# Kernel optimization log

Hardware: AMD Instinct MI355X
Metric: run time of the kernel (lower is better)

Reference implementation:

```python
import jax, jax.numpy as jnp
import numpy as np

DIM = 512
HEADS = 8
DIM_HEAD = 64
INNER = HEADS * DIM_HEAD  # 512


def setup_inputs() -> dict:
    key = jax.random.key(0)
    k1, k2, k3, k4 = jax.random.split(key, 4)
    x = jax.random.normal(k1, (2, 4096, DIM), dtype=jnp.float32)
    w_qkv = jax.random.normal(k2, (DIM, INNER * 3), dtype=jnp.float32) * (DIM ** -0.5)
    w_out = jax.random.normal(k3, (INNER, DIM), dtype=jnp.float32) * (INNER ** -0.5)
    b_out = jnp.zeros((DIM,), dtype=jnp.float32)
    temperature = jnp.asarray(np.log(DIM_HEAD ** -0.5), dtype=jnp.float32)
    return {"x": x, "w_qkv": w_qkv, "w_out": w_out, "b_out": b_out,
            "temperature": temperature}


def reference(x, w_qkv, w_out, b_out, temperature):
    b, n, _ = x.shape
    qkv = jnp.einsum('bnd,de->bne', x, w_qkv)            # [b,n,3*inner]
    q, k, v = jnp.split(qkv, 3, axis=-1)
    # 'b n (h d) -> b h n d'
    def to_heads(t):
        return t.reshape(b, n, HEADS, DIM_HEAD).transpose(0, 2, 1, 3)
    q, k, v = map(to_heads, (q, k, v))
    scale = jnp.exp(temperature)
    dots = jnp.einsum('bhid,bhjd->bhij', q, k) * scale   # [b,h,n,n]
    mask_value = -jnp.asarray(np.finfo(np.float32).max, dtype=dots.dtype)
    eye = jnp.eye(n, dtype=bool)
    dots = jnp.where(eye, mask_value, dots)
    attn = jax.nn.softmax(dots, axis=-1)
    out = jnp.einsum('bhij,bhjd->bhid', attn, v)         # [b,h,n,d]
    out = out.transpose(0, 2, 1, 3).reshape(b, n, INNER)  # 'b h n d -> b n (h d)'
    return jnp.einsum('bni,io->bno', out, w_out) + b_out
```

## Files before the change

kernel.cpp:

```cpp
#include <hip/hip_runtime.h>

typedef __bf16 bf16x8 __attribute__((ext_vector_type(8)));
typedef float  f32x4  __attribute__((ext_vector_type(4)));
typedef unsigned short u16;
typedef unsigned int   u32;

#define MFMA(a,b,c) __builtin_amdgcn_mfma_f32_16x16x32_bf16((a),(b),(c),0,0,0)

__device__ __forceinline__ u16 f2bf(float f){
    u32 u = __builtin_bit_cast(u32, f);
    u += 0x7FFFu + ((u >> 16) & 1u);
    return (u16)(u >> 16);
}

typedef __attribute__((address_space(3))) u32 lds32_t;
typedef __attribute__((address_space(1))) u32 glb32_t;

__device__ __forceinline__ void gll16(const u16* g, u16* l){
    __builtin_amdgcn_global_load_lds((const glb32_t*)g, (lds32_t*)l, 16, 0, 0);
}

__global__ __launch_bounds__(256) void cvt_x_kernel(const float* __restrict__ in,
                                                    u16* __restrict__ out, int n8){
    int i = blockIdx.x * 256 + threadIdx.x;
    if (i >= n8) return;
    const float4* p = (const float4*)in + (size_t)i * 2;
    float4 a = p[0], b = p[1];
    u16 r[8] = { f2bf(a.x), f2bf(a.y), f2bf(a.z), f2bf(a.w),
                 f2bf(b.x), f2bf(b.y), f2bf(b.z), f2bf(b.w) };
    *((uint4*)out + i) = *(const uint4*)r;
}

__global__ __launch_bounds__(256) void tcvt_kernel(const float* __restrict__ in,
                                                   u16* __restrict__ out, int R, int C){
    __shared__ float tile[32][33];
    int c0 = blockIdx.x * 32, r0 = blockIdx.y * 32;
    int tx = threadIdx.x & 31, ty = threadIdx.x >> 5;
    #pragma unroll
    for (int i = 0; i < 32; i += 8)
        tile[ty + i][tx] = in[(size_t)(r0 + ty + i) * C + c0 + tx];
    __syncthreads();
    #pragma unroll
    for (int i = 0; i < 32; i += 8)
        out[(size_t)(c0 + ty + i) * R + r0 + tx] = f2bf(tile[tx][ty + i]);
}

__device__ __forceinline__ void gemm_core(const u16* __restrict__ A, const u16* __restrict__ Bt,
                                          int brow, int bcol, u16* ldsA, u16* ldsB,
                                          f32x4 acc[4][4]){
    const int t = threadIdx.x;
    const int lane = t & 63, wave = t >> 6;
    const int l16 = lane & 15, lg = lane >> 4;
    const int wrow = (wave & 1) << 6, wcol = (wave >> 1) << 6;

    for (int ks = 0; ks < 8; ++ks){
        if (ks) __syncthreads();
        #pragma unroll
        for (int iss = 0; iss < 4; ++iss){
            int chunk = iss * 256 + t;
            int row = chunk >> 3, c = chunk & 7;
            int sw = (c ^ (row & 7)) << 3;
            gll16(A  + (size_t)(brow + row) * 512 + ks * 64 + sw,
                  ldsA + (size_t)(iss * 256 + wave * 64) * 8);
            gll16(Bt + (size_t)(bcol + row) * 512 + ks * 64 + sw,
                  ldsB + (size_t)(iss * 256 + wave * 64) * 8);
        }
        __syncthreads();
        #pragma unroll
        for (int kc = 0; kc < 2; ++kc){
            bf16x8 af[4], bfr[4];
            #pragma unroll
            for (int m = 0; m < 4; ++m){
                int r = wrow + 16 * m + l16;
                af[m] = *(const bf16x8*)(ldsA + r * 64 + (((kc * 4 + lg) ^ (l16 & 7)) << 3));
            }
            #pragma unroll
            for (int n = 0; n < 4; ++n){
                int r = wcol + 16 * n + l16;
                bfr[n] = *(const bf16x8*)(ldsB + r * 64 + (((kc * 4 + lg) ^ (l16 & 7)) << 3));
            }
            #pragma unroll
            for (int m = 0; m < 4; ++m)
                #pragma unroll
                for (int n = 0; n < 4; ++n)
                    acc[m][n] = MFMA(af[m], bfr[n], acc[m][n]);
        }
    }
}

__global__ __launch_bounds__(256) void gemm_qkv_kernel(const u16* __restrict__ A, const u16* __restrict__ Bt,
                                                       u16* __restrict__ qws, u16* __restrict__ kws,
                                                       u16* __restrict__ vtws,
                                                       const float* __restrict__ temp){
    __shared__ u16 ldsA[128 * 64];
    __shared__ u16 ldsB[128 * 64];
    const f32x4 vzero = {0.f, 0.f, 0.f, 0.f};
    f32x4 acc[4][4];
    #pragma unroll
    for (int m = 0; m < 4; ++m)
        #pragma unroll
        for (int n = 0; n < 4; ++n) acc[m][n] = vzero;

    int brow = blockIdx.x * 128, bcol = blockIdx.y * 128;
    gemm_core(A, Bt, brow, bcol, ldsA, ldsB, acc);

    const int t = threadIdx.x, lane = t & 63, wave = t >> 6;
    const int l16 = lane & 15, lg = lane >> 4;
    const int wrow = (wave & 1) << 6, wcol = (wave >> 1) << 6;
    const int s = bcol >> 9;

    if (s < 2){
        u16* dst = (s == 0) ? qws : kws;
        float qs = (s == 0) ? (__expf(temp[0]) * 1.44269504f) : 1.0f;
        #pragma unroll
        for (int n = 0; n < 4; ++n){
            int e = (bcol & 511) + wcol + 16 * n + l16;
            int h = e >> 6, d = e & 63;
            #pragma unroll
            for (int m = 0; m < 4; ++m)
                #pragma unroll
                for (int r = 0; r < 4; ++r){
                    int mg = brow + wrow + 16 * m + 4 * lg + r;
                    int b = mg >> 12, nn = mg & 4095;
                    dst[(((size_t)(b * 8 + h) * 4096 + nn) << 6) + d] = f2bf(acc[m][n][r] * qs);
                }
        }
    } else {
        #pragma unroll
        for (int n = 0; n < 4; ++n){
            int e = (bcol & 511) + wcol + 16 * n + l16;
            int h = e >> 6, d = e & 63;
            #pragma unroll
            for (int m = 0; m < 4; ++m)
                #pragma unroll
                for (int r = 0; r < 4; ++r){
                    int mg = brow + wrow + 16 * m + 4 * lg + r;
                    int b = mg >> 12, nn = mg & 4095;
                    vtws[((size_t)((b * 8 + h) * 64 + d) << 12) + nn] = f2bf(acc[m][n][r]);
                }
        }
    }
}

__global__ __launch_bounds__(256) void attn_kernel(const u16* __restrict__ q, const u16* __restrict__ k,
                                                   const u16* __restrict__ vt, u16* __restrict__ aout){
    __shared__ u16 Kl[64 * 64];
    __shared__ u16 Vl[64 * 64];
    __shared__ u16 Pl[4][16 * 72];
    const int bid = blockIdx.x;
    const int qt = bid & 63, bh = bid >> 6;
    const int t = threadIdx.x, lane = t & 63, wave = t >> 6;
    const int l16 = lane & 15, lg = lane >> 4;

    const int qrow = qt * 64 + wave * 16 + l16;
    const u16* qb = q + (((size_t)bh * 4096 + qrow) << 6);
    bf16x8 qa[2];
    qa[0] = *(const bf16x8*)(qb + (lg << 3));
    qa[1] = *(const bf16x8*)(qb + 32 + (lg << 3));

    const f32x4 vzero = {0.f, 0.f, 0.f, 0.f};
    f32x4 o[4];
    #pragma unroll
    for (int i = 0; i < 4; ++i) o[i] = vzero;
    float mv = -INFINITY, ls = 0.f;

    for (int kb = 0; kb < 4096; kb += 64){
        __syncthreads();
        #pragma unroll
        for (int iss = 0; iss < 2; ++iss){
            int chunk = iss * 256 + t;
            int row = chunk >> 3, c = chunk & 7;
            int sw = (c ^ (row & 7)) << 3;
            gll16(k  + (((size_t)bh * 4096 + kb + row) << 6) + sw,
                  Kl + (iss * 256 + wave * 64) * 8);
            gll16(vt + ((size_t)(bh * 64 + row) << 12) + kb + sw,
                  Vl + (iss * 256 + wave * 64) * 8);
        }
        __syncthreads();

        f32x4 s[4];
        #pragma unroll
        for (int fc = 0; fc < 4; ++fc){
            s[fc] = vzero;
            #pragma unroll
            for (int dc = 0; dc < 2; ++dc){
                bf16x8 kf = *(const bf16x8*)(Kl + (16 * fc + l16) * 64 +
                                             (((dc * 4 + lg) ^ (l16 & 7)) << 3));
                s[fc] = MFMA(kf, qa[dc], s[fc]);
            }
        }
        if (kb == qt * 64){
            int dd = wave * 16 + l16;
            #pragma unroll
            for (int fc = 0; fc < 4; ++fc)
                #pragma unroll
                for (int r = 0; r < 4; ++r)
                    if (dd == fc * 16 + 4 * lg + r) s[fc][r] = -1e30f;
        }
        float pm0 = fmaxf(fmaxf(s[0][0], s[0][1]), fmaxf(s[0][2], s[0][3]));
        float pm1 = fmaxf(fmaxf(s[1][0], s[1][1]), fmaxf(s[1][2], s[1][3]));
        float pm2 = fmaxf(fmaxf(s[2][0], s[2][1]), fmaxf(s[2][2], s[2][3]));
        float pm3 = fmaxf(fmaxf(s[3][0], s[3][1]), fmaxf(s[3][2], s[3][3]));
        float pm = fmaxf(fmaxf(pm0, pm1), fmaxf(pm2, pm3));
        pm = fmaxf(pm, __shfl_xor(pm, 16));
        pm = fmaxf(pm, __shfl_xor(pm, 32));
        if (__any(pm > mv + 8.0f)){
            float mn = fmaxf(mv, pm);
            float al = __builtin_amdgcn_exp2f(mv - mn);
            mv = mn;
            ls *= al;
            #pragma unroll
            for (int dn = 0; dn < 4; ++dn)
                #pragma unroll
                for (int r = 0; r < 4; ++r) o[dn][r] *= al;
        }
        float rs0 = 0.f, rs1 = 0.f;
        #pragma unroll
        for (int fc = 0; fc < 4; ++fc){
            u32 pb[4];
            #pragma unroll
            for (int r = 0; r < 4; ++r){
                float p = __builtin_amdgcn_exp2f(s[fc][r] - mv);
                u32 bb = __builtin_bit_cast(u32, p) & 0xffff0000u;
                pb[r] = bb;
                if (r & 1) rs1 += __builtin_bit_cast(float, bb);
                else       rs0 += __builtin_bit_cast(float, bb);
            }
            uint2 w;
            w.x = __builtin_amdgcn_perm(pb[1], pb[0], 0x07060302u);
            w.y = __builtin_amdgcn_perm(pb[3], pb[2], 0x07060302u);
            *(uint2*)&Pl[wave][l16 * 72 + 16 * fc + 4 * lg] = w;
        }
        float rs = rs0 + rs1;
        rs += __shfl_xor(rs, 16);
        rs += __shfl_xor(rs, 32);
        ls += rs;
        #pragma unroll
        for (int kc = 0; kc < 2; ++kc){
            bf16x8 pa = *(const bf16x8*)(&Pl[wave][l16 * 72 + kc * 32 + lg * 8]);
            #pragma unroll
            for (int dn = 0; dn < 4; ++dn){
                bf16x8 vf = *(const bf16x8*)(Vl + (16 * dn + l16) * 64 +
                                             (((kc * 4 + lg) ^ (l16 & 7)) << 3));
                o[dn] = MFMA(vf, pa, o[dn]);
            }
        }
    }
    const int b = bh >> 3, h = bh & 7;
    const float inv = __builtin_amdgcn_rcpf(ls);
    const int n = qt * 64 + wave * 16 + l16;
    size_t base = ((size_t)b * 4096 + n) * 512 + h * 64;
    #pragma unroll
    for (int dn = 0; dn < 4; ++dn){
        u16 e0 = f2bf(o[dn][0] * inv), e1 = f2bf(o[dn][1] * inv);
        u16 e2 = f2bf(o[dn][2] * inv), e3 = f2bf(o[dn][3] * inv);
        uint2 w;
        w.x = (u32)e0 | ((u32)e1 << 16);
        w.y = (u32)e2 | ((u32)e3 << 16);
        *(uint2*)&aout[base + dn * 16 + lg * 4] = w;
    }
}

__global__ __launch_bounds__(256) void gemm_out_kernel(const u16* __restrict__ A, const u16* __restrict__ Bt,
                                                       const float* __restrict__ bias,
                                                       float* __restrict__ out){
    __shared__ u16 ldsA[128 * 64];
    __shared__ u16 ldsB[128 * 64];
    const f32x4 vzero = {0.f, 0.f, 0.f, 0.f};
    f32x4 acc[4][4];
    #pragma unroll
    for (int m = 0; m < 4; ++m)
        #pragma unroll
        for (int n = 0; n < 4; ++n) acc[m][n] = vzero;

    int brow = blockIdx.x * 128, bcol = blockIdx.y * 128;
    gemm_core(A, Bt, brow, bcol, ldsA, ldsB, acc);

    const int t = threadIdx.x, lane = t & 63, wave = t >> 6;
    const int l16 = lane & 15, lg = lane >> 4;
    const int wrow = (wave & 1) << 6, wcol = (wave >> 1) << 6;
    #pragma unroll
    for (int n = 0; n < 4; ++n){
        int e = bcol + wcol + 16 * n + l16;
        float bv = bias[e];
        #pragma unroll
        for (int m = 0; m < 4; ++m)
            #pragma unroll
            for (int r = 0; r < 4; ++r){
                int mg = brow + wrow + 16 * m + 4 * lg + r;
                out[(size_t)mg * 512 + e] = acc[m][n][r] + bv;
            }
    }
}

extern "C" void kernel_launch(void* const* d_in, const int* in_sizes, int n_in,
                              void* d_out, int out_size, void* d_ws, size_t ws_size,
                              hipStream_t stream){
    (void)in_sizes; (void)n_in; (void)out_size; (void)ws_size;
    const float* x     = (const float*)d_in[0];
    const float* w_qkv = (const float*)d_in[1];
    const float* w_out = (const float*)d_in[2];
    const float* b_out = (const float*)d_in[3];
    const float* temp  = (const float*)d_in[4];
    float* out = (float*)d_out;

    u16* ws   = (u16*)d_ws;
    u16* xbf  = ws;
    u16* wqt  = xbf + 8192 * 512;
    u16* wot  = wqt + 1536 * 512;
    u16* qws  = wot + 512 * 512;
    u16* kws  = qws + 16 * 4096 * 64;
    u16* vtws = kws + 16 * 4096 * 64;
    u16* aout = xbf;

    cvt_x_kernel<<<2048, 256, 0, stream>>>(x, xbf, 8192 * 512 / 8);
    tcvt_kernel<<<dim3(48, 16), 256, 0, stream>>>(w_qkv, wqt, 512, 1536);
    tcvt_kernel<<<dim3(16, 16), 256, 0, stream>>>(w_out, wot, 512, 512);
    gemm_qkv_kernel<<<dim3(64, 12), 256, 0, stream>>>(xbf, wqt, qws, kws, vtws, temp);
    attn_kernel<<<1024, 256, 0, stream>>>(qws, kws, vtws, aout);
    gemm_out_kernel<<<dim3(64, 4), 256, 0, stream>>>(aout, wot, b_out, out);
}
```

Baseline: 187.4 us.

## Double-buffer K/V tiles in attention and raise wave priority around MFMAs

The attention kernel now keeps two LDS buffers for K and V. It issues the global-to-LDS loads for the next 64-key tile before computing on the current one, so the loads overlap the QK^T, softmax and PV work, and it drops to one barrier per iteration. It also wraps both MFMA blocks in s_setprio(1)/s_setprio(0) to favour waves issuing matrix instructions. In exchange, LDS use roughly doubles for K/V, which may reduce occupancy. The loads must also finish before the end-of-iteration barrier, so the overlap depends on how the waitcnt is placed.

```diff
diff --git a/kernel.cpp b/kernel.cpp
--- a/kernel.cpp
+++ b/kernel.cpp
@@ -5,7 +5,7 @@
 typedef unsigned short u16;
 typedef unsigned int   u32;
 
-#define MFMA(a,b,c) __builtin_amdgcn_mfma_f32_16x16x32_bf16((a),(b),(c),0,0,0)
+#define MFMA16(a,b,c) __builtin_amdgcn_mfma_f32_16x16x32_bf16((a),(b),(c),0,0,0)
 
 __device__ __forceinline__ u16 f2bf(float f){
     u32 u = __builtin_bit_cast(u32, f);
@@ -83,7 +83,7 @@
             for (int m = 0; m < 4; ++m)
                 #pragma unroll
                 for (int n = 0; n < 4; ++n)
-                    acc[m][n] = MFMA(af[m], bfr[n], acc[m][n]);
+                    acc[m][n] = MFMA16(af[m], bfr[n], acc[m][n]);
         }
     }
 }
@@ -144,14 +144,29 @@
 
 __global__ __launch_bounds__(256) void attn_kernel(const u16* __restrict__ q, const u16* __restrict__ k,
                                                    const u16* __restrict__ vt, u16* __restrict__ aout){
-    __shared__ u16 Kl[64 * 64];
-    __shared__ u16 Vl[64 * 64];
+    __shared__ u16 Kl[2][64 * 64];
+    __shared__ u16 Vl[2][64 * 64];
     __shared__ u16 Pl[4][16 * 72];
     const int bid = blockIdx.x;
     const int qt = bid & 63, bh = bid >> 6;
     const int t = threadIdx.x, lane = t & 63, wave = t >> 6;
     const int l16 = lane & 15, lg = lane >> 4;
 
+    auto stage = [&](int buf, int kb){
+        #pragma unroll
+        for (int iss = 0; iss < 2; ++iss){
+            int chunk = iss * 256 + t;
+            int row = chunk >> 3, c = chunk & 7;
+            int sw = (c ^ (row & 7)) << 3;
+            gll16(k  + (((size_t)bh * 4096 + kb + row) << 6) + sw,
+                  &Kl[buf][(iss * 256 + wave * 64) * 8]);
+            gll16(vt + ((size_t)(bh * 64 + row) << 12) + kb + sw,
+                  &Vl[buf][(iss * 256 + wave * 64) * 8]);
+        }
+    };
+
+    stage(0, 0);
+
     const int qrow = qt * 64 + wave * 16 + l16;
     const u16* qb = q + (((size_t)bh * 4096 + qrow) << 6);
     bf16x8 qa[2];
@@ -164,31 +179,28 @@
     for (int i = 0; i < 4; ++i) o[i] = vzero;
     float mv = -INFINITY, ls = 0.f;
 
-    for (int kb = 0; kb < 4096; kb += 64){
-        __syncthreads();
-        #pragma unroll
-        for (int iss = 0; iss < 2; ++iss){
-            int chunk = iss * 256 + t;
-            int row = chunk >> 3, c = chunk & 7;
-            int sw = (c ^ (row & 7)) << 3;
-            gll16(k  + (((size_t)bh * 4096 + kb + row) << 6) + sw,
-                  Kl + (iss * 256 + wave * 64) * 8);
-            gll16(vt + ((size_t)(bh * 64 + row) << 12) + kb + sw,
-                  Vl + (iss * 256 + wave * 64) * 8);
-        }
-        __syncthreads();
+    __syncthreads();
+
+    for (int it = 0; it < 64; ++it){
+        const int cur = it & 1;
+        if (it < 63) stage(cur ^ 1, (it + 1) << 6);
+        const u16* Kc = Kl[cur];
+        const u16* Vc = Vl[cur];
+        const int kb = it << 6;
 
         f32x4 s[4];
+        __builtin_amdgcn_s_setprio(1);
         #pragma unroll
         for (int fc = 0; fc < 4; ++fc){
             s[fc] = vzero;
             #pragma unroll
             for (int dc = 0; dc < 2; ++dc){
-                bf16x8 kf = *(const bf16x8*)(Kl + (16 * fc + l16) * 64 +
+                bf16x8 kf = *(const bf16x8*)(Kc + (16 * fc + l16) * 64 +
                                              (((dc * 4 + lg) ^ (l16 & 7)) << 3));
-                s[fc] = MFMA(kf, qa[dc], s[fc]);
-            }
-        }
+                s[fc] = MFMA16(kf, qa[dc], s[fc]);
+            }
+        }
+        __builtin_amdgcn_s_setprio(0);
         if (kb == qt * 64){
             int dd = wave * 16 + l16;
             #pragma unroll
@@ -235,16 +247,19 @@
         rs += __shfl_xor(rs, 16);
         rs += __shfl_xor(rs, 32);
         ls += rs;
+        __builtin_amdgcn_s_setprio(1);
         #pragma unroll
         for (int kc = 0; kc < 2; ++kc){
             bf16x8 pa = *(const bf16x8*)(&Pl[wave][l16 * 72 + kc * 32 + lg * 8]);
             #pragma unroll
             for (int dn = 0; dn < 4; ++dn){
-                bf16x8 vf = *(const bf16x8*)(Vl + (16 * dn + l16) * 64 +
+                bf16x8 vf = *(const bf16x8*)(Vc + (16 * dn + l16) * 64 +
                                              (((kc * 4 + lg) ^ (l16 & 7)) << 3));
-                o[dn] = MFMA(vf, pa, o[dn]);
-            }
-        }
+                o[dn] = MFMA16(vf, pa, o[dn]);
+            }
+        }
+        __builtin_amdgcn_s_setprio(0);
+        __syncthreads();
     }
     const int b = bh >> 3, h = bh & 7;
     const float inv = __builtin_amdgcn_rcpf(ls);
```

Result: slower. 219.5 us (+17.2%).

## Compute softmax row sums via MFMA with ones vector and use packed bf16 convert

Applied to the files above, without the earlier changes.

Replaces the per-lane row-sum accumulation and cross-lane shuffles with an extra MFMA that multiplies a ones vector by the P tile, yielding the denominator in the matrix unit. Exponentials are now packed to bf16 with a hardware v_cvt_pk_bf16_f32 (round-to-nearest instead of truncation), the row max uses three-input max chains, and MFMA sections are wrapped in s_setprio to favour matrix issue. This moves VALU and shuffle work onto the MFMA pipe at the cost of one extra MFMA per k-chunk.

```diff
diff --git a/kernel.cpp b/kernel.cpp
--- a/kernel.cpp
+++ b/kernel.cpp
@@ -5,12 +5,22 @@
 typedef unsigned short u16;
 typedef unsigned int   u32;
 
-#define MFMA(a,b,c) __builtin_amdgcn_mfma_f32_16x16x32_bf16((a),(b),(c),0,0,0)
+#define MFMA16(a,b,c) __builtin_amdgcn_mfma_f32_16x16x32_bf16((a),(b),(c),0,0,0)
 
 __device__ __forceinline__ u16 f2bf(float f){
     u32 u = __builtin_bit_cast(u32, f);
     u += 0x7FFFu + ((u >> 16) & 1u);
     return (u16)(u >> 16);
+}
+
+__device__ __forceinline__ u32 cvt_pk_bf16(float lo, float hi){
+    u32 r;
+    asm("v_cvt_pk_bf16_f32 %0, %1, %2" : "=v"(r) : "v"(lo), "v"(hi));
+    return r;
+}
+
+__device__ __forceinline__ float max3f(float a, float b, float c){
+    return fmaxf(fmaxf(a, b), c);
 }
 
 typedef __attribute__((address_space(3))) u32 lds32_t;
@@ -83,7 +93,7 @@
             for (int m = 0; m < 4; ++m)
                 #pragma unroll
                 for (int n = 0; n < 4; ++n)
-                    acc[m][n] = MFMA(af[m], bfr[n], acc[m][n]);
+                    acc[m][n] = MFMA16(af[m], bfr[n], acc[m][n]);
         }
     }
 }
@@ -158,11 +168,15 @@
     qa[0] = *(const bf16x8*)(qb + (lg << 3));
     qa[1] = *(const bf16x8*)(qb + 32 + (lg << 3));
 
+    const uint4 ow = {0x3F803F80u, 0x3F803F80u, 0x3F803F80u, 0x3F803F80u};
+    const bf16x8 ones = __builtin_bit_cast(bf16x8, ow);
+
     const f32x4 vzero = {0.f, 0.f, 0.f, 0.f};
     f32x4 o[4];
+    f32x4 o4 = vzero;
     #pragma unroll
     for (int i = 0; i < 4; ++i) o[i] = vzero;
-    float mv = -INFINITY, ls = 0.f;
+    float mv = -INFINITY;
 
     for (int kb = 0; kb < 4096; kb += 64){
         __syncthreads();
@@ -179,6 +193,7 @@
         __syncthreads();
 
         f32x4 s[4];
+        __builtin_amdgcn_s_setprio(1);
         #pragma unroll
         for (int fc = 0; fc < 4; ++fc){
             s[fc] = vzero;
@@ -186,9 +201,10 @@
             for (int dc = 0; dc < 2; ++dc){
                 bf16x8 kf = *(const bf16x8*)(Kl + (16 * fc + l16) * 64 +
                                              (((dc * 4 + lg) ^ (l16 & 7)) << 3));
-                s[fc] = MFMA(kf, qa[dc], s[fc]);
-            }
-        }
+            s[fc] = MFMA16(kf, qa[dc], s[fc]);
+            }
+        }
+        __builtin_amdgcn_s_setprio(0);
         if (kb == qt * 64){
             int dd = wave * 16 + l16;
             #pragma unroll
@@ -197,57 +213,51 @@
                 for (int r = 0; r < 4; ++r)
                     if (dd == fc * 16 + 4 * lg + r) s[fc][r] = -1e30f;
         }
-        float pm0 = fmaxf(fmaxf(s[0][0], s[0][1]), fmaxf(s[0][2], s[0][3]));
-        float pm1 = fmaxf(fmaxf(s[1][0], s[1][1]), fmaxf(s[1][2], s[1][3]));
-        float pm2 = fmaxf(fmaxf(s[2][0], s[2][1]), fmaxf(s[2][2], s[2][3]));
-        float pm3 = fmaxf(fmaxf(s[3][0], s[3][1]), fmaxf(s[3][2], s[3][3]));
-        float pm = fmaxf(fmaxf(pm0, pm1), fmaxf(pm2, pm3));
+        float g0 = max3f(s[0][0], s[0][1], s[0][2]);
+        float g1 = max3f(s[0][3], s[1][0], s[1][1]);
+        float g2 = max3f(s[1][2], s[1][3], s[2][0]);
+        float g3 = max3f(s[2][1], s[2][2], s[2][3]);
+        float g4 = max3f(s[3][0], s[3][1], s[3][2]);
+        float pm = fmaxf(max3f(max3f(g0, g1, g2), g3, g4), s[3][3]);
         pm = fmaxf(pm, __shfl_xor(pm, 16));
         pm = fmaxf(pm, __shfl_xor(pm, 32));
         if (__any(pm > mv + 8.0f)){
             float mn = fmaxf(mv, pm);
             float al = __builtin_amdgcn_exp2f(mv - mn);
             mv = mn;
-            ls *= al;
+            o4 *= al;
             #pragma unroll
             for (int dn = 0; dn < 4; ++dn)
                 #pragma unroll
                 for (int r = 0; r < 4; ++r) o[dn][r] *= al;
         }
-        float rs0 = 0.f, rs1 = 0.f;
         #pragma unroll
         for (int fc = 0; fc < 4; ++fc){
-            u32 pb[4];
-            #pragma unroll
-            for (int r = 0; r < 4; ++r){
-                float p = __builtin_amdgcn_exp2f(s[fc][r] - mv);
-                u32 bb = __builtin_bit_cast(u32, p) & 0xffff0000u;
-                pb[r] = bb;
-                if (r & 1) rs1 += __builtin_bit_cast(float, bb);
-                else       rs0 += __builtin_bit_cast(float, bb);
-            }
+            float p0 = __builtin_amdgcn_exp2f(s[fc][0] - mv);
+            float p1 = __builtin_amdgcn_exp2f(s[fc][1] - mv);
+            float p2 = __builtin_amdgcn_exp2f(s[fc][2] - mv);
+            float p3 = __builtin_amdgcn_exp2f(s[fc][3] - mv);
             uint2 w;
-            w.x = __builtin_amdgcn_perm(pb[1], pb[0], 0x07060302u);
-            w.y = __builtin_amdgcn_perm(pb[3], pb[2], 0x07060302u);
+            w.x = cvt_pk_bf16(p0, p1);
+            w.y = cvt_pk_bf16(p2, p3);
             *(uint2*)&Pl[wave][l16 * 72 + 16 * fc + 4 * lg] = w;
         }
-        float rs = rs0 + rs1;
-        rs += __shfl_xor(rs, 16);
-        rs += __shfl_xor(rs, 32);
-        ls += rs;
+        __builtin_amdgcn_s_setprio(1);
         #pragma unroll
         for (int kc = 0; kc < 2; ++kc){
             bf16x8 pa = *(const bf16x8*)(&Pl[wave][l16 * 72 + kc * 32 + lg * 8]);
+            o4 = MFMA16(ones, pa, o4);
             #pragma unroll
             for (int dn = 0; dn < 4; ++dn){
                 bf16x8 vf = *(const bf16x8*)(Vl + (16 * dn + l16) * 64 +
                                              (((kc * 4 + lg) ^ (l16 & 7)) << 3));
-                o[dn] = MFMA(vf, pa, o[dn]);
-            }
-        }
+                o[dn] = MFMA16(vf, pa, o[dn]);
+            }
+        }
+        __builtin_amdgcn_s_setprio(0);
     }
     const int b = bh >> 3, h = bh & 7;
-    const float inv = __builtin_amdgcn_rcpf(ls);
+    const float inv = __builtin_amdgcn_rcpf(o4[0]);
     const int n = qt * 64 + wave * 16 + l16;
     size_t base = ((size_t)b * 4096 + n) * 512 + h * 64;
     #pragma unroll
```

New measurement: 170.2 us. 1.1x faster.
